# Kernel tuning notes

Hardware: AMD Instinct MI355X
Metric: run time of the kernel (lower is better)

The kernel has to match this reference:

```python
import jax, jax.numpy as jnp
import numpy as np
from jax import lax

L, D, V, T = 12, 1024, 50277, 1024
F4 = 4 * D


def setup_inputs() -> dict:
    key = jax.random.key(0)
    ks = jax.random.split(key, 20)
    s = 0.02  # weight scale keeps k (exp argument) well-conditioned
    n = lambda k, shape, scale=s: jax.random.normal(k, shape, dtype=jnp.float32) * scale
    u = lambda k, shape: jax.random.uniform(k, shape, dtype=jnp.float32)
    return {
        "tokens": jax.random.randint(ks[0], (T,), 0, V, dtype=jnp.int32),
        "emb": n(ks[1], (V, D), 1.0),
        "ln0_w": jnp.ones((D,), jnp.float32), "ln0_b": jnp.zeros((D,), jnp.float32),
        "ln1_w": jnp.ones((L, D), jnp.float32), "ln1_b": jnp.zeros((L, D), jnp.float32),
        "ln2_w": jnp.ones((L, D), jnp.float32), "ln2_b": jnp.zeros((L, D), jnp.float32),
        "tmk": u(ks[2], (L, D)), "tmv": u(ks[3], (L, D)), "tmr": u(ks[4], (L, D)),
        "tmk_ffn": u(ks[5], (L, D)), "tmr_ffn": u(ks[6], (L, D)),
        "time_first": n(ks[7], (L, D), 0.5),
        "time_decay": -jnp.exp(n(ks[8], (L, D), 0.5)),  # __init__: -exp(raw)
        "att_kw": n(ks[9], (L, D, D)), "att_vw": n(ks[10], (L, D, D)),
        "att_rw": n(ks[11], (L, D, D)), "att_ow": n(ks[12], (L, D, D)),
        "ffn_kw": n(ks[13], (L, D, F4)), "ffn_vw": n(ks[14], (L, F4, D)),
        "ffn_rw": n(ks[15], (L, D, D)),
        "lnout_w": jnp.ones((D,), jnp.float32), "lnout_b": jnp.zeros((D,), jnp.float32),
        "head": n(ks[16], (V, D)),
    }


def _ln(x, w, b):
    mu = jnp.mean(x, -1, keepdims=True)
    var = jnp.var(x, -1, keepdims=True)
    return (x - mu) / jnp.sqrt(var + 1e-5) * w + b


def _shift(x):  # token shift: prepend zero state row (state init is zeros)
    return jnp.concatenate([jnp.zeros_like(x[:1]), x[:-1]], axis=0)


def _wkv(k, v, tf, td):  # k,v: [T,D]; aa/bb/pp scan with running-max exp trick
    init = (jnp.zeros_like(k[0]), jnp.zeros_like(k[0]), jnp.full_like(k[0], -1e30))
    def step(c, kv):
        aa, bb, pp = c
        kt, vt = kv
        ww = tf + kt
        p = jnp.maximum(pp, ww)
        e1 = jnp.exp(pp - p); e2 = jnp.exp(ww - p)
        out = (e1 * aa + e2 * vt) / (e1 * bb + e2)
        ww2 = pp + td
        p2 = jnp.maximum(ww2, kt)
        e1 = jnp.exp(ww2 - p2); e2 = jnp.exp(kt - p2)
        return (e1 * aa + e2 * vt, e1 * bb + e2, p2), out
    _, out = lax.scan(step, init, (k, v))
    return out


def reference(tokens, emb, ln0_w, ln0_b, ln1_w, ln1_b, ln2_w, ln2_b, tmk, tmv, tmr,
              tmk_ffn, tmr_ffn, time_first, time_decay, att_kw, att_vw, att_rw, att_ow,
              ffn_kw, ffn_vw, ffn_rw, lnout_w, lnout_b, head):
    x = _ln(emb[tokens], ln0_w, ln0_b)  # [T,D]; ln0 applied to emb rows as in __init__
    for i in range(L):
        # time-mix (attention) block
        xn = _ln(x, ln1_w[i], ln1_b[i])
        xx = _shift(xn)
        xk = xn * tmk[i] + xx * (1 - tmk[i])
        xv = xn * tmv[i] + xx * (1 - tmv[i])
        xr = xn * tmr[i] + xx * (1 - tmr[i])
        r = jax.nn.sigmoid(xr @ att_rw[i])
        k = xk @ att_kw[i]
        v = xv @ att_vw[i]
        wkv = _wkv(k, v, time_first[i], time_decay[i])
        x = x + (r * wkv) @ att_ow[i]
        # channel-mix (ffn) block
        xn = _ln(x, ln2_w[i], ln2_b[i])
        xx = _shift(xn)
        xk = xn * tmk_ffn[i] + xx * (1 - tmk_ffn[i])
        xr = xn * tmr_ffn[i] + xx * (1 - tmr_ffn[i])
        rf = jax.nn.sigmoid(xr @ ffn_rw[i])
        kf = jnp.square(jax.nn.relu(xk @ ffn_kw[i]))
        x = x + rf * (kf @ ffn_vw[i])
    xo = _ln(x[-1], lnout_w, lnout_b)
    return head @ xo  # logits [V]
```

## Files before the change

kernel.cpp:

```cpp
#include <hip/hip_runtime.h>

#define Tn 1024
#define Dn 1024
#define Ln 12
#define F4n 4096
#define Vn 50277
#define TDn (Tn*Dn)
#define MEG 1048576
#define SEG 16
#define NSEG 64

typedef __attribute__((ext_vector_type(4))) float f4;
typedef __attribute__((ext_vector_type(16))) float f32x16;
typedef __attribute__((ext_vector_type(8))) short short8;
typedef unsigned short u16;
typedef unsigned int u32;
typedef __attribute__((ext_vector_type(4))) u16 us4;

#define ASG __attribute__((address_space(1)))
#define ASL __attribute__((address_space(3)))

__device__ __forceinline__ u16 f2b(float x){
  u32 u = __float_as_uint(x);
  return (u16)((u + 0x7fffu + ((u >> 16) & 1u)) >> 16);
}

__device__ __forceinline__ f4 blockReduce4(f4 v){
  __shared__ f4 s[4];
  int lane = threadIdx.x & 63, w = threadIdx.x >> 6;
#pragma unroll
  for(int o = 32; o; o >>= 1){
    v.x += __shfl_xor(v.x, o);
    v.y += __shfl_xor(v.y, o);
    v.z += __shfl_xor(v.z, o);
    v.w += __shfl_xor(v.w, o);
  }
  if(lane == 0) s[w] = v;
  __syncthreads();
  return s[0] + s[1] + s[2] + s[3];
}

struct ConvArgs {
  const float* s0; const float* s1; const float* s2; const float* s3;
  const float* skw;
  const float* svw;
  const float* srw;
  u16* dst;
};
__global__ __launch_bounds__(256) void conv_k(ConvArgs a){
  __shared__ __align__(16) u16 t[64][68];
  int b = blockIdx.x, tid = threadIdx.x;
  const float* src; u16* dst; int K, N, tk, tn;
  if(b < 1024){
    int m = b >> 8, bt = b & 255;
    src = (m==0)?a.s0:((m==1)?a.s1:((m==2)?a.s2:a.s3));
    dst = a.dst + (size_t)m*MEG; K=1024; N=1024; tk=bt>>4; tn=bt&15;
  } else if(b < 2048){
    int bt = b-1024; src=a.skw; dst=a.dst+(size_t)4*MEG; K=1024; N=4096; tk=bt>>6; tn=bt&63;
  } else if(b < 3072){
    int bt = b-2048; src=a.svw; dst=a.dst+(size_t)8*MEG; K=4096; N=1024; tk=bt>>4; tn=bt&15;
  } else {
    int bt = b-3072; src=a.srw; dst=a.dst+(size_t)12*MEG; K=1024; N=1024; tk=bt>>4; tn=bt&15;
  }
  int rr0 = tid >> 4, c4 = (tid & 15)*4;
#pragma unroll
  for(int p=0;p<4;p++){
    int r = p*16 + rr0;
    f4 v = *(const f4*)(src + (size_t)(tk*64+r)*N + tn*64 + c4);
    us4 h; h[0]=f2b(v.x); h[1]=f2b(v.y); h[2]=f2b(v.z); h[3]=f2b(v.w);
    *(us4*)&t[r][c4] = h;
  }
  __syncthreads();
  int q = tid & 3, n = tid >> 2;
  int k0 = q*16;
  union { short8 v; u16 h[8]; } o0, o1;
#pragma unroll
  for(int j=0;j<8;j++){ o0.h[j]=t[k0+j][n]; o1.h[j]=t[k0+8+j][n]; }
  u16* dp = dst + (size_t)(tn*64+n)*K + tk*64 + k0;
  *(short8*)dp       = o0.v;
  *(short8*)(dp + 8) = o1.v;
}

__global__ __launch_bounds__(256) void embed_ln0_k(
    const int* __restrict__ tok, const float* __restrict__ emb,
    const float* __restrict__ w, const float* __restrict__ b,
    float* __restrict__ x){
  int t = blockIdx.x, tid = threadIdx.x;
  const f4* src = (const f4*)(emb + (size_t)tok[t] * Dn);
  f4 v = src[tid];
  f4 st;
  st.x = v.x+v.y+v.z+v.w;
  st.y = v.x*v.x+v.y*v.y+v.z*v.z+v.w*v.w;
  st.z = 0.f; st.w = 0.f;
  f4 red = blockReduce4(st);
  float mu = red.x * (1.0f/Dn);
  float rs = rsqrtf(red.y * (1.0f/Dn) - mu*mu + 1e-5f);
  f4 wv = ((const f4*)w)[tid], bv = ((const f4*)b)[tid];
  f4 o;
  o.x = (v.x-mu)*rs*wv.x + bv.x;
  o.y = (v.y-mu)*rs*wv.y + bv.y;
  o.z = (v.z-mu)*rs*wv.z + bv.z;
  o.w = (v.w-mu)*rs*wv.w + bv.w;
  ((f4*)(x + (size_t)t*Dn))[tid] = o;
}

__global__ __launch_bounds__(256) void ln_mix_att_k(
    const float* __restrict__ x,
    const float* __restrict__ lw, const float* __restrict__ lb,
    const float* __restrict__ tk, const float* __restrict__ tv, const float* __restrict__ tr,
    u16* __restrict__ xkvr){
  int t = blockIdx.x, tid = threadIdx.x;
  f4 cur = ((const f4*)(x + (size_t)t*Dn))[tid];
  f4 prv; prv.x=0.f; prv.y=0.f; prv.z=0.f; prv.w=0.f;
  if(t > 0) prv = ((const f4*)(x + (size_t)(t-1)*Dn))[tid];
  f4 st;
  st.x = cur.x+cur.y+cur.z+cur.w;
  st.y = cur.x*cur.x+cur.y*cur.y+cur.z*cur.z+cur.w*cur.w;
  st.z = prv.x+prv.y+prv.z+prv.w;
  st.w = prv.x*prv.x+prv.y*prv.y+prv.z*prv.z+prv.w*prv.w;
  f4 red = blockReduce4(st);
  float muc = red.x*(1.f/Dn), rsc = rsqrtf(red.y*(1.f/Dn)-muc*muc+1e-5f);
  float mup = red.z*(1.f/Dn), rsp = rsqrtf(red.w*(1.f/Dn)-mup*mup+1e-5f);
  f4 wv=((const f4*)lw)[tid], bv=((const f4*)lb)[tid];
  f4 kv=((const f4*)tk)[tid], vv=((const f4*)tv)[tid], rv=((const f4*)tr)[tid];
  us4 ok, ov, orr;
  float xn, xp;
#define MIX3(j, cj, pj, wj, bj, kj, vj, rj) \
  xn = (cj - muc)*rsc*wj + bj; \
  xp = (t>0) ? ((pj - mup)*rsp*wj + bj) : 0.f; \
  ok[j]  = f2b(xn*kj + xp*(1.f-kj)); \
  ov[j]  = f2b(xn*vj + xp*(1.f-vj)); \
  orr[j] = f2b(xn*rj + xp*(1.f-rj));
  MIX3(0, cur.x, prv.x, wv.x, bv.x, kv.x, vv.x, rv.x)
  MIX3(1, cur.y, prv.y, wv.y, bv.y, kv.y, vv.y, rv.y)
  MIX3(2, cur.z, prv.z, wv.z, bv.z, kv.z, vv.z, rv.z)
  MIX3(3, cur.w, prv.w, wv.w, bv.w, kv.w, vv.w, rv.w)
#undef MIX3
  size_t o0 = (size_t)t*Dn + tid*4;
  *(us4*)(xkvr + o0)         = ok;
  *(us4*)(xkvr + TDn + o0)   = ov;
  *(us4*)(xkvr + 2*TDn + o0) = orr;
}

__global__ __launch_bounds__(256) void ln_mix_ffn_k(
    const float* __restrict__ x,
    const float* __restrict__ lw, const float* __restrict__ lb,
    const float* __restrict__ tk, const float* __restrict__ tr,
    u16* __restrict__ xkr){
  int t = blockIdx.x, tid = threadIdx.x;
  f4 cur = ((const f4*)(x + (size_t)t*Dn))[tid];
  f4 prv; prv.x=0.f; prv.y=0.f; prv.z=0.f; prv.w=0.f;
  if(t > 0) prv = ((const f4*)(x + (size_t)(t-1)*Dn))[tid];
  f4 st;
  st.x = cur.x+cur.y+cur.z+cur.w;
  st.y = cur.x*cur.x+cur.y*cur.y+cur.z*cur.z+cur.w*cur.w;
  st.z = prv.x+prv.y+prv.z+prv.w;
  st.w = prv.x*prv.x+prv.y*prv.y+prv.z*prv.z+prv.w*prv.w;
  f4 red = blockReduce4(st);
  float muc = red.x*(1.f/Dn), rsc = rsqrtf(red.y*(1.f/Dn)-muc*muc+1e-5f);
  float mup = red.z*(1.f/Dn), rsp = rsqrtf(red.w*(1.f/Dn)-mup*mup+1e-5f);
  f4 wv=((const f4*)lw)[tid], bv=((const f4*)lb)[tid];
  f4 kv=((const f4*)tk)[tid], rv=((const f4*)tr)[tid];
  us4 ok, orr;
  float xn, xp;
#define MIX2(j, cj, pj, wj, bj, kj, rj) \
  xn = (cj - muc)*rsc*wj + bj; \
  xp = (t>0) ? ((pj - mup)*rsp*wj + bj) : 0.f; \
  ok[j]  = f2b(xn*kj + xp*(1.f-kj)); \
  orr[j] = f2b(xn*rj + xp*(1.f-rj));
  MIX2(0, cur.x, prv.x, wv.x, bv.x, kv.x, rv.x)
  MIX2(1, cur.y, prv.y, wv.y, bv.y, kv.y, rv.y)
  MIX2(2, cur.z, prv.z, wv.z, bv.z, kv.z, rv.z)
  MIX2(3, cur.w, prv.w, wv.w, bv.w, kv.w, rv.w)
#undef MIX2
  size_t o0 = (size_t)t*Dn + tid*4;
  *(us4*)(xkr + o0)       = ok;
  *(us4*)(xkr + TDn + o0) = orr;
}

__global__ __launch_bounds__(256) void wkv_seg_k(
    const float* __restrict__ kb, const float* __restrict__ vb,
    const float* __restrict__ tdp,
    float* __restrict__ sega, float* __restrict__ segb, float* __restrict__ segp){
  int ch = blockIdx.x*256 + threadIdx.x;
  int g = blockIdx.y;
  int t0 = g*SEG;
  float td = tdp[ch];
  float kk[SEG], vv[SEG];
#pragma unroll
  for(int j=0;j<SEG;j++){
    kk[j] = kb[(size_t)(t0+j)*Dn + ch];
    vv[j] = vb[(size_t)(t0+j)*Dn + ch];
  }
  float aa=0.f, bb=0.f, pp=-1e30f;
#pragma unroll
  for(int j=0;j<SEG;j++){
    float ww2 = pp + td;
    float p2 = fmaxf(ww2, kk[j]);
    float e1 = __expf(ww2-p2), e2 = __expf(kk[j]-p2);
    aa = e1*aa + e2*vv[j]; bb = e1*bb + e2; pp = p2;
  }
  size_t o = (size_t)g*Dn + ch;
  sega[o] = aa; segb[o] = bb; segp[o] = pp;
}

__global__ __launch_bounds__(256) void wkv_scan_k(
    const float* __restrict__ sega, const float* __restrict__ segb, const float* __restrict__ segp,
    const float* __restrict__ tdp,
    float* __restrict__ prea, float* __restrict__ preb, float* __restrict__ prep){
  int ch = blockIdx.x*256 + threadIdx.x;
  float Std = tdp[ch] * (float)SEG;
  float a=0.f, b=0.f, p=-1e30f;
  for(int g=0; g<NSEG; g++){
    size_t o = (size_t)g*Dn + ch;
    prea[o]=a; preb[o]=b; prep[o]=p;
    float ag=sega[o], bg=segb[o], qg=segp[o];
    float psh = p + Std;
    float pn = fmaxf(psh, qg);
    float eo = __expf(psh-pn), en = __expf(qg-pn);
    a = eo*a + en*ag; b = eo*b + en*bg; p = pn;
  }
}

__global__ __launch_bounds__(256) void wkv_out_k(
    const float* __restrict__ kb, const float* __restrict__ vb, const float* __restrict__ rb,
    const float* __restrict__ tfp, const float* __restrict__ tdp,
    const float* __restrict__ prea, const float* __restrict__ preb, const float* __restrict__ prep,
    u16* __restrict__ att_in){
  int ch = blockIdx.x*256 + threadIdx.x;
  int g = blockIdx.y;
  int t0 = g*SEG;
  float tf = tfp[ch], td = tdp[ch];
  size_t so = (size_t)g*Dn + ch;
  float aa = prea[so], bb = preb[so], pp = prep[so];
  float kk[SEG], vv[SEG], rr[SEG];
#pragma unroll
  for(int j=0;j<SEG;j++){
    kk[j]=kb[(size_t)(t0+j)*Dn+ch];
    vv[j]=vb[(size_t)(t0+j)*Dn+ch];
    rr[j]=rb[(size_t)(t0+j)*Dn+ch];
  }
#pragma unroll
  for(int j=0;j<SEG;j++){
    float kt=kk[j], vt=vv[j];
    float ww = tf + kt;
    float p = fmaxf(pp, ww);
    float e1 = __expf(pp-p), e2 = __expf(ww-p);
    float out = __fdividef(e1*aa+e2*vt, e1*bb+e2);
    float sig = __fdividef(1.f, 1.f+__expf(-rr[j]));
    att_in[(size_t)(t0+j)*Dn+ch] = f2b(sig*out);
    float ww2 = pp+td;
    float p2 = fmaxf(ww2,kt);
    e1 = __expf(ww2-p2); e2 = __expf(kt-p2);
    aa = e1*aa+e2*vt; bb = e1*bb+e2; pp = p2;
  }
}

template<int EPI, int KSTEP, int WAVES>
__global__ __launch_bounds__(WAVES*64) void gemm_k(
    const u16* __restrict__ A, size_t ldA, size_t strideA,
    const u16* __restrict__ Bt, size_t ldB, size_t strideB,
    int K, int N,
    float* __restrict__ Cf, size_t strideC, u16* __restrict__ Cb,
    const float* __restrict__ aux){
  extern __shared__ __align__(16) u16 ldsd[];
  constexpr int RPC = 512/KSTEP;
  constexpr int LPR = 64/RPC;
  constexpr int NCH = KSTEP/8;
  constexpr int NQ  = NCH/WAVES;
  constexpr int WKB = 2*KSTEP/WAVES;
  constexpr int NS  = WKB/32;
  const int tid = threadIdx.x;
  const int l = tid & 63, w = tid >> 6;
  const int z = blockIdx.z;
  const int row0 = blockIdx.y*64, col0 = blockIdx.x*64;

  const u16* bA = A  + (size_t)z*strideA + (size_t)row0*ldA;
  const u16* bB = Bt + (size_t)z*strideB + (size_t)col0*ldB;

  int offA[NQ], offB[NQ], ldso[NQ];
#pragma unroll
  for(int q=0;q<NQ;q++){
    int ch = q*WAVES + w;
    int r  = ch*RPC + l/LPR;
    int phys = (l%LPR)*16;
    int kk = ((phys ^ ((r&15)<<4)) >> 1);
    offA[q] = r*(int)ldA + kk;
    offB[q] = r*(int)ldB + kk;
    ldso[q] = ch*512;
  }
  int foff[2][NS];
#pragma unroll
  for(int i=0;i<2;i++){
    int row = i*32 + (l&31);
#pragma unroll
    for(int s=0;s<NS;s++){
      int c = w*WKB + s*32 + ((l>>5)*16);
      foff[i][s] = row*KSTEP + ((c ^ ((row&15)<<4)) >> 1);
    }
  }

  f32x16 acc[2][2];
#pragma unroll
  for(int i=0;i<2;i++)
#pragma unroll
    for(int j=0;j<2;j++)
#pragma unroll
      for(int e=0;e<16;e++) acc[i][j][e] = 0.f;

  u16* ldsA0 = ldsd;
  u16* ldsB0 = ldsd + 64*KSTEP;
  u16* ldsA1 = ldsd + 2*64*KSTEP;
  u16* ldsB1 = ldsd + 3*64*KSTEP;

#define STAGE(LA, LB) do{ \
  _Pragma("unroll") \
  for(int q=0;q<NQ;q++){ \
    __builtin_amdgcn_global_load_lds((ASG const void*)(const void*)(bA + offA[q]), (ASL void*)(void*)((LA) + ldso[q]), 16, 0, 0); \
    __builtin_amdgcn_global_load_lds((ASG const void*)(const void*)(bB + offB[q]), (ASL void*)(void*)((LB) + ldso[q]), 16, 0, 0); \
  } \
  bA += KSTEP; bB += KSTEP; }while(0)

  const int nss = K / KSTEP;
  STAGE(ldsA0, ldsB0);
  __syncthreads();
  int buf = 0;
  for(int ss=0; ss<nss; ss++){
    if(ss+1 < nss){
      if(buf) STAGE(ldsA0, ldsB0); else STAGE(ldsA1, ldsB1);
    }
    const u16* La = buf ? ldsA1 : ldsA0;
    const u16* Lb = buf ? ldsB1 : ldsB0;
#pragma unroll
    for(int s=0;s<NS;s++){
      short8 a0 = *(const short8*)(La + foff[0][s]);
      short8 a1 = *(const short8*)(La + foff[1][s]);
      short8 b0 = *(const short8*)(Lb + foff[0][s]);
      short8 b1 = *(const short8*)(Lb + foff[1][s]);
      acc[0][0] = __builtin_amdgcn_mfma_f32_32x32x16_bf16(a0, b0, acc[0][0], 0, 0, 0);
      acc[0][1] = __builtin_amdgcn_mfma_f32_32x32x16_bf16(a0, b1, acc[0][1], 0, 0, 0);
      acc[1][0] = __builtin_amdgcn_mfma_f32_32x32x16_bf16(a1, b0, acc[1][0], 0, 0, 0);
      acc[1][1] = __builtin_amdgcn_mfma_f32_32x32x16_bf16(a1, b1, acc[1][1], 0, 0, 0);
    }
    __syncthreads();
    buf ^= 1;
  }
#undef STAGE

  float* red = (float*)ldsd;
  if(w > 0){
#pragma unroll
    for(int i=0;i<2;i++)
#pragma unroll
      for(int j=0;j<2;j++)
#pragma unroll
        for(int reg=0;reg<16;reg++){
          int rr_ = (reg&3) + 8*(reg>>2) + 4*(l>>5);
          red[(size_t)(w-1)*4096 + (size_t)(i*32 + rr_)*64 + j*32 + (l&31)] = acc[i][j][reg];
        }
  }
  __syncthreads();
  if(w == 0){
#pragma unroll
    for(int i=0;i<2;i++)
#pragma unroll
      for(int j=0;j<2;j++)
#pragma unroll
        for(int reg=0;reg<16;reg++){
          int rr_ = (reg&3) + 8*(reg>>2) + 4*(l>>5);
          size_t lidx = (size_t)(i*32 + rr_)*64 + j*32 + (l&31);
          float v = acc[i][j][reg];
#pragma unroll
          for(int p=0;p<WAVES-1;p++) v += red[(size_t)p*4096 + lidx];
          int grow = row0 + i*32 + rr_;
          int gcol = col0 + j*32 + (l&31);
          size_t idx = (size_t)grow*N + gcol;
          if constexpr(EPI==0){ Cf[(size_t)z*strideC + idx] = v; }
          else if constexpr(EPI==1){ float t_ = v>0.f ? v : 0.f; Cb[idx] = f2b(t_*t_); }
          else if constexpr(EPI==2){ Cf[idx] += v; }
          else { float s_ = __fdividef(1.f, 1.f+__expf(-aux[idx])); Cf[idx] += s_*v; }
        }
  }
}

__global__ __launch_bounds__(256) void lnout_k(
    const float* __restrict__ x, const float* __restrict__ w, const float* __restrict__ b,
    float* __restrict__ xo){
  int tid = threadIdx.x;
  f4 v = ((const f4*)(x + (size_t)(Tn-1)*Dn))[tid];
  f4 st;
  st.x = v.x+v.y+v.z+v.w;
  st.y = v.x*v.x+v.y*v.y+v.z*v.z+v.w*v.w;
  st.z = 0.f; st.w = 0.f;
  f4 red = blockReduce4(st);
  float mu = red.x*(1.f/Dn);
  float rs = rsqrtf(red.y*(1.f/Dn) - mu*mu + 1e-5f);
  f4 wv = ((const f4*)w)[tid], bv = ((const f4*)b)[tid];
  f4 o;
  o.x = (v.x-mu)*rs*wv.x + bv.x;
  o.y = (v.y-mu)*rs*wv.y + bv.y;
  o.z = (v.z-mu)*rs*wv.z + bv.z;
  o.w = (v.w-mu)*rs*wv.w + bv.w;
  ((f4*)xo)[tid] = o;
}

__global__ __launch_bounds__(256) void head_k(
    const float* __restrict__ head, const float* __restrict__ xo, float* __restrict__ out){
  __shared__ f4 sxo[256];
  int tid = threadIdx.x;
  sxo[tid] = ((const f4*)xo)[tid];
  __syncthreads();
  int w = tid >> 6, lane = tid & 63;
  int row = blockIdx.x*4 + w;
  if(row < Vn){
    const f4* hr = (const f4*)(head + (size_t)row*Dn);
    float s = 0.f;
#pragma unroll
    for(int i=0;i<4;i++){
      f4 h = hr[i*64 + lane];
      f4 xv = sxo[i*64 + lane];
      s += h.x*xv.x + h.y*xv.y + h.z*xv.z + h.w*xv.w;
    }
#pragma unroll
    for(int o=32;o;o>>=1) s += __shfl_xor(s, o);
    if(lane == 0) out[row] = s;
  }
}

extern "C" void kernel_launch(void* const* d_in, const int* in_sizes, int n_in,
                              void* d_out, int out_size, void* d_ws, size_t ws_size,
                              hipStream_t stream) {
  (void)in_sizes; (void)n_in; (void)out_size; (void)ws_size;
  const int*   tokens   = (const int*)  d_in[0];
  const float* emb      = (const float*)d_in[1];
  const float* ln0_w    = (const float*)d_in[2];
  const float* ln0_b    = (const float*)d_in[3];
  const float* ln1_w    = (const float*)d_in[4];
  const float* ln1_b    = (const float*)d_in[5];
  const float* ln2_w    = (const float*)d_in[6];
  const float* ln2_b    = (const float*)d_in[7];
  const float* tmk      = (const float*)d_in[8];
  const float* tmv      = (const float*)d_in[9];
  const float* tmr      = (const float*)d_in[10];
  const float* tmk_ffn  = (const float*)d_in[11];
  const float* tmr_ffn  = (const float*)d_in[12];
  const float* tfirst   = (const float*)d_in[13];
  const float* tdecay   = (const float*)d_in[14];
  const float* att_kw   = (const float*)d_in[15];
  const float* att_vw   = (const float*)d_in[16];
  const float* att_rw   = (const float*)d_in[17];
  const float* att_ow   = (const float*)d_in[18];
  const float* ffn_kw   = (const float*)d_in[19];
  const float* ffn_vw   = (const float*)d_in[20];
  const float* ffn_rw   = (const float*)d_in[21];
  const float* lnoutw   = (const float*)d_in[22];
  const float* lnoutb   = (const float*)d_in[23];
  const float* headw    = (const float*)d_in[24];
  float* logits = (float*)d_out;

  char* wsb = (char*)d_ws;
  size_t off = 0;
  auto carve = [&](size_t bytes)->void*{
    void* p = wsb + off;
    off += (bytes + 255) & ~(size_t)255;
    return p;
  };
  float* x      = (float*)carve((size_t)TDn*4);
  u16*   xkvr   = (u16*)  carve((size_t)3*TDn*2);
  float* kvr    = (float*)carve((size_t)3*TDn*4);
  u16*   att_in = (u16*)  carve((size_t)TDn*2);
  u16*   xkr    = (u16*)  carve((size_t)2*TDn*2);
  u16*   kf     = (u16*)  carve((size_t)Tn*F4n*2);
  float* rf     = (float*)carve((size_t)TDn*4);
  float* xo     = (float*)carve((size_t)Dn*4);
  u16*   wbt    = (u16*)  carve((size_t)13*MEG*2);
  float* sega   = (float*)carve((size_t)NSEG*Dn*4);
  float* segb   = (float*)carve((size_t)NSEG*Dn*4);
  float* segp   = (float*)carve((size_t)NSEG*Dn*4);
  float* prea   = (float*)carve((size_t)NSEG*Dn*4);
  float* preb   = (float*)carve((size_t)NSEG*Dn*4);
  float* prep   = (float*)carve((size_t)NSEG*Dn*4);

  embed_ln0_k<<<Tn, 256, 0, stream>>>(tokens, emb, ln0_w, ln0_b, x);

  for(int i=0;i<Ln;i++){
    size_t dd = (size_t)i*Dn*Dn;
    ConvArgs ca;
    ca.s0 = att_kw+dd; ca.s1 = att_vw+dd; ca.s2 = att_rw+dd; ca.s3 = att_ow+dd;
    ca.skw = ffn_kw+(size_t)i*Dn*F4n; ca.svw = ffn_vw+(size_t)i*F4n*Dn; ca.srw = ffn_rw+dd;
    ca.dst = wbt;
    conv_k<<<3328, 256, 0, stream>>>(ca);

    ln_mix_att_k<<<Tn, 256, 0, stream>>>(x, ln1_w+i*Dn, ln1_b+i*Dn,
                                         tmk+i*Dn, tmv+i*Dn, tmr+i*Dn, xkvr);
    gemm_k<0,128,2><<<dim3(16,16,3), 128, 65536, stream>>>(
        xkvr, Dn, (size_t)TDn, wbt, Dn, (size_t)MEG, Dn, Dn,
        kvr, (size_t)TDn, nullptr, nullptr);
    wkv_seg_k<<<dim3(4,NSEG), 256, 0, stream>>>(kvr, kvr+TDn, tdecay+i*Dn, sega, segb, segp);
    wkv_scan_k<<<4, 256, 0, stream>>>(sega, segb, segp, tdecay+i*Dn, prea, preb, prep);
    wkv_out_k<<<dim3(4,NSEG), 256, 0, stream>>>(kvr, kvr+TDn, kvr+2*TDn,
                                                tfirst+i*Dn, tdecay+i*Dn,
                                                prea, preb, prep, att_in);
    gemm_k<2,256,4><<<dim3(16,16,1), 256, 131072, stream>>>(
        att_in, Dn, 0, wbt+(size_t)3*MEG, Dn, 0, Dn, Dn,
        x, 0, nullptr, nullptr);
    ln_mix_ffn_k<<<Tn, 256, 0, stream>>>(x, ln2_w+i*Dn, ln2_b+i*Dn,
                                         tmk_ffn+i*Dn, tmr_ffn+i*Dn, xkr);
    gemm_k<1,128,2><<<dim3(64,16,1), 128, 65536, stream>>>(
        xkr, Dn, 0, wbt+(size_t)4*MEG, Dn, 0, Dn, F4n,
        nullptr, 0, kf, nullptr);
    gemm_k<0,256,4><<<dim3(16,16,1), 256, 131072, stream>>>(
        xkr+TDn, Dn, 0, wbt+(size_t)12*MEG, Dn, 0, Dn, Dn,
        rf, 0, nullptr, nullptr);
    gemm_k<3,256,4><<<dim3(16,16,1), 256, 131072, stream>>>(
        kf, F4n, 0, wbt+(size_t)8*MEG, F4n, 0, F4n, Dn,
        x, 0, nullptr, rf);
  }

  lnout_k<<<1, 256, 0, stream>>>(x, lnoutw, lnoutb, xo);
  head_k<<<(Vn+3)/4, 256, 0, stream>>>(headw, xo, logits);
}
```

Baseline: 1.878 ms.

## Add dedicated 128x128 double-buffered GEMM for FFN key projection

Replaces the generic gemm_k call for the FFN key projection (T x 4D output, relu-squared bf16 epilogue) with a specialized kernel. It uses 128x128 output tiles over 4 waves, each wave computing 64x64, and the K dimension is split into 64-wide stages. Global-to-LDS loads are double-buffered so the next stage streams in while the current one runs through MFMA. The aim is more data reuse per block and load/compute overlap without split-K reduction through LDS. The trade-offs are fewer blocks (256) and higher register use per thread.

```diff
diff --git a/kernel.cpp b/kernel.cpp
--- a/kernel.cpp
+++ b/kernel.cpp
@@ -383,6 +383,107 @@
   }
 }
 
+__global__ __launch_bounds__(256) void gemm_fk_k(
+    const u16* __restrict__ A,
+    const u16* __restrict__ Bt,
+    u16* __restrict__ Cb){
+  extern __shared__ __align__(16) u16 ldsd[];
+  constexpr int KS = 64;
+  const int tid = threadIdx.x;
+  const int l = tid & 63, w = tid >> 6;
+  const int wm = (w>>1)*64, wn = (w&1)*64;
+  const int row0 = blockIdx.y*128, col0 = blockIdx.x*128;
+
+  const u16* bA = A  + (size_t)row0*Dn;
+  const u16* bB = Bt + (size_t)col0*Dn;
+
+  int offA[4], offB[4], ldso[4];
+#pragma unroll
+  for(int q=0;q<4;q++){
+    int ch = q*4 + w;
+    int r  = ch*8 + (l>>3);
+    int kk = ((((l&7)*16) ^ ((l>>3)<<4)) >> 1);
+    offA[q] = r*Dn + kk;
+    offB[q] = r*Dn + kk;
+    ldso[q] = ch*512;
+  }
+  int foffA[2][4], foffB[2][4];
+#pragma unroll
+  for(int i=0;i<2;i++){
+    int ar = wm + i*32 + (l&31);
+    int br = wn + i*32 + (l&31);
+#pragma unroll
+    for(int s=0;s<4;s++){
+      int c = s*32 + ((l>>5)*16);
+      foffA[i][s] = ar*KS + ((c ^ ((ar&7)<<4)) >> 1);
+      foffB[i][s] = br*KS + ((c ^ ((br&7)<<4)) >> 1);
+    }
+  }
+
+  f32x16 acc[2][2];
+#pragma unroll
+  for(int i=0;i<2;i++)
+#pragma unroll
+    for(int j=0;j<2;j++)
+#pragma unroll
+      for(int e=0;e<16;e++) acc[i][j][e] = 0.f;
+
+  u16* ldsA0 = ldsd;
+  u16* ldsB0 = ldsd + 8192;
+  u16* ldsA1 = ldsd + 16384;
+  u16* ldsB1 = ldsd + 24576;
+
+#define STAGE(LA, LB) do{ \
+  _Pragma("unroll") \
+  for(int q=0;q<4;q++){ \
+    __builtin_amdgcn_global_load_lds((ASG const void*)(const void*)(bA + offA[q]), (ASL void*)(void*)((LA) + ldso[q]), 16, 0, 0); \
+    __builtin_amdgcn_global_load_lds((ASG const void*)(const void*)(bB + offB[q]), (ASL void*)(void*)((LB) + ldso[q]), 16, 0, 0); \
+  } \
+  bA += KS; bB += KS; }while(0)
+
+  STAGE(ldsA0, ldsB0);
+  __syncthreads();
+  int buf = 0;
+#pragma unroll 1
+  for(int ss=0; ss<16; ss++){
+    if(ss+1 < 16){
+      if(buf) STAGE(ldsA0, ldsB0); else STAGE(ldsA1, ldsB1);
+    }
+    const u16* La = buf ? ldsA1 : ldsA0;
+    const u16* Lb = buf ? ldsB1 : ldsB0;
+#pragma unroll
+    for(int s=0;s<4;s++){
+      short8 a0 = *(const short8*)(La + foffA[0][s]);
+      short8 a1 = *(const short8*)(La + foffA[1][s]);
+      short8 b0 = *(const short8*)(Lb + foffB[0][s]);
+      short8 b1 = *(const short8*)(Lb + foffB[1][s]);
+      acc[0][0] = __builtin_amdgcn_mfma_f32_32x32x16_bf16(a0, b0, acc[0][0], 0, 0, 0);
+      acc[0][1] = __builtin_amdgcn_mfma_f32_32x32x16_bf16(a0, b1, acc[0][1], 0, 0, 0);
+      acc[1][0] = __builtin_amdgcn_mfma_f32_32x32x16_bf16(a1, b0, acc[1][0], 0, 0, 0);
+      acc[1][1] = __builtin_amdgcn_mfma_f32_32x32x16_bf16(a1, b1, acc[1][1], 0, 0, 0);
+    }
+    __syncthreads();
+    buf ^= 1;
+  }
+#undef STAGE
+
+#pragma unroll
+  for(int i=0;i<2;i++){
+#pragma unroll
+    for(int j=0;j<2;j++){
+#pragma unroll
+      for(int reg=0;reg<16;reg++){
+        int rr_ = (reg&3) + 8*(reg>>2) + 4*(l>>5);
+        int grow = row0 + wm + i*32 + rr_;
+        int gcol = col0 + wn + j*32 + (l&31);
+        float v = acc[i][j][reg];
+        float t_ = v>0.f ? v : 0.f;
+        Cb[(size_t)grow*F4n + gcol] = f2b(t_*t_);
+      }
+    }
+  }
+}
+
 __global__ __launch_bounds__(256) void lnout_k(
     const float* __restrict__ x, const float* __restrict__ w, const float* __restrict__ b,
     float* __restrict__ xo){
@@ -506,9 +607,7 @@
         x, 0, nullptr, nullptr);
     ln_mix_ffn_k<<<Tn, 256, 0, stream>>>(x, ln2_w+i*Dn, ln2_b+i*Dn,
                                          tmk_ffn+i*Dn, tmr_ffn+i*Dn, xkr);
-    gemm_k<1,128,2><<<dim3(64,16,1), 128, 65536, stream>>>(
-        xkr, Dn, 0, wbt+(size_t)4*MEG, Dn, 0, Dn, F4n,
-        nullptr, 0, kf, nullptr);
+    gemm_fk_k<<<dim3(32,8), 256, 65536, stream>>>(xkr, wbt+(size_t)4*MEG, kf);
     gemm_k<0,256,4><<<dim3(16,16,1), 256, 131072, stream>>>(
         xkr+TDn, Dn, 0, wbt+(size_t)12*MEG, Dn, 0, Dn, Dn,
         rf, 0, nullptr, nullptr);
```

New measurement: 1.799 ms. -4.2%, faster.
